# Optimization experiments

Hardware: AMD Instinct MI355X
Metric: run time of the kernel (lower is better)

## Reference

```python
import jax, jax.numpy as jnp
import numpy as np
from jax.scipy.special import logsumexp

B, L, S, C = 8, 2048, 2048, 256
ITERS = 20

def setup_inputs() -> dict:
    key = jax.random.key(0)
    k0, k1 = jax.random.split(key)
    feat_c0 = jax.random.normal(k0, (B, L, C), dtype=jnp.float32)
    feat_c1 = jax.random.normal(k1, (B, S, C), dtype=jnp.float32)
    bin_score = jnp.ones((), dtype=jnp.float32)  # init_bin_score = 1.0
    return {"feat_c0": feat_c0, "feat_c1": feat_c1, "bin_score": bin_score}

def _uniform_prior(b, m, n):
    # build_uniform_prior: norm = -log(m+n); log_mu/[log_nu] over augmented rows/cols
    fm, fn = jnp.float32(m), jnp.float32(n)
    norm = -jnp.log(fm + fn)
    log_mu = jnp.concatenate([jnp.full((m,), norm, jnp.float32), (jnp.log(fn) + norm)[None]])
    log_nu = jnp.concatenate([jnp.full((n,), norm, jnp.float32), (jnp.log(fm) + norm)[None]])
    log_mu = jnp.broadcast_to(log_mu[None], (b, m + 1))
    log_nu = jnp.broadcast_to(log_nu[None], (b, n + 1))
    return log_mu, log_nu, norm

def _log_sinkhorn(Z, log_mu, log_nu, iters):
    u0 = jnp.zeros_like(log_mu)
    v0 = jnp.zeros_like(log_nu)
    def body(carry, _):
        u, v = carry
        u = log_mu - logsumexp(Z + v[:, None, :], axis=2)  # [B, M+1]
        v = log_nu - logsumexp(Z + u[:, :, None], axis=1)  # [B, N+1]
        return (u, v), None
    (u, v), _ = jax.lax.scan(body, (u0, v0), None, length=iters)
    return Z + u[:, :, None] + v[:, None, :]

def reference(feat_c0, feat_c1, bin_score):
    b, m, n = feat_c0.shape[0], feat_c0.shape[1], feat_c1.shape[1]
    scores = jnp.einsum('blc,bsc->bls', feat_c0, feat_c1)  # [B, M, N]
    # augment with dustbin row/col
    bins0 = jnp.broadcast_to(bin_score, (b, m, 1))
    bins1 = jnp.broadcast_to(bin_score, (b, 1, n))
    alpha = jnp.broadcast_to(bin_score, (b, 1, 1))
    Zin = jnp.concatenate([
        jnp.concatenate([scores, bins0], axis=-1),
        jnp.concatenate([bins1, alpha], axis=-1),
    ], axis=1)  # [B, M+1, N+1]
    log_mu, log_nu, norm = _uniform_prior(b, m, n)
    Z = _log_sinkhorn(Zin, log_mu, log_nu, ITERS)
    return Z - norm
```

## Files before the change

kernel.cpp:

```cpp
#include <hip/hip_runtime.h>

#define Bn 8
#define Mn 2048
#define Nn 2048
#define Cn 256
#define Np1 2049
#define Mp1 2049
#define UVS 2056
#define SINK_ITERS 20
#define NORM   (-8.3177661667193428f)
#define LOGBIN (-0.6931471805599453f)
#define LOG2E  (1.4426950408889634f)
#define LN2    (0.6931471805599453f)
#define NORM2  (-12.0f)
#define LOGBIN2 (-1.0f)
#define PNORM  (8.3177661667193428f)

#define EXP2(x) __builtin_amdgcn_exp2f(x)
#define LOG2(x) __builtin_amdgcn_logf(x)

typedef __bf16 v8bf __attribute__((ext_vector_type(8)));
typedef float  v4f  __attribute__((ext_vector_type(4)));
typedef unsigned short v8u __attribute__((ext_vector_type(8)));

__device__ __forceinline__ float bf2f(unsigned short h){
  return __uint_as_float(((unsigned)h) << 16);
}
__device__ __forceinline__ unsigned short f2bf(float f){
  unsigned u = __float_as_uint(f);
  return (unsigned short)((u + 0x7FFFu + ((u >> 16) & 1u)) >> 16);
}
__device__ __forceinline__ float ldS(const float* p){ return *p; }
__device__ __forceinline__ float ldS(const unsigned short* p){ return bf2f(*p); }
__device__ __forceinline__ void  stS(float* p, float x){ *p = x; }
__device__ __forceinline__ void  stS(unsigned short* p, float x){ *p = f2bf(x); }

__device__ __forceinline__ void ons(float x, float& m, float& s){
  if (x <= m) { s += __expf(x - m); }
  else        { s = s * __expf(m - x) + 1.0f; m = x; }
}
__device__ __forceinline__ void comb(float& m, float& s, float m2, float s2){
  if (m2 <= m) { s += s2 * __expf(m2 - m); }
  else         { s = s * __expf(m - m2) + s2; m = m2; }
}

__global__ void __launch_bounds__(256) conv_k(
    const float* __restrict__ in, unsigned short* __restrict__ out, float scale)
{
  size_t idx = (size_t)blockIdx.x * 256 + threadIdx.x;
  const float* p = in + idx * 8;
  v4f a = *(const v4f*)p;
  v4f c = *(const v4f*)(p + 4);
  v8u o;
  #pragma unroll
  for (int e = 0; e < 4; ++e){ o[e] = f2bf(a[e] * scale); o[e+4] = f2bf(c[e] * scale); }
  *(v8u*)(out + idx * 8) = o;
}

__global__ void __launch_bounds__(256) gemm_bt(
    const unsigned short* __restrict__ A, const unsigned short* __restrict__ Bm,
    unsigned short* __restrict__ S, unsigned short* __restrict__ ST)
{
  __shared__ unsigned short lt[4][64][65];
  int wid  = (blockIdx.x * 256 + threadIdx.x) >> 6;
  int w    = (threadIdx.x >> 6) & 3;
  int lane = threadIdx.x & 63;
  int b  = wid >> 10;
  int tt = wid & 1023;
  int i0 = (tt >> 5) << 6;
  int j0 = (tt & 31) << 6;
  int ln = lane & 15, qd = lane >> 4;
  const unsigned short* Ab = A  + (size_t)b * Mn * Cn;
  const unsigned short* Bb = Bm + (size_t)b * Nn * Cn;

  v4f acc[4][4];
  #pragma unroll
  for (int r = 0; r < 4; ++r)
    #pragma unroll
    for (int c = 0; c < 4; ++c)
      #pragma unroll
      for (int e = 0; e < 4; ++e) acc[r][c][e] = 0.0f;

  #pragma unroll
  for (int k0 = 0; k0 < Cn; k0 += 32){
    int kk = k0 + qd * 8;
    v8bf af[4], bfr[4];
    #pragma unroll
    for (int r = 0; r < 4; ++r)
      af[r] = *(const v8bf*)(const void*)(Ab + (size_t)(i0 + r*16 + ln) * Cn + kk);
    #pragma unroll
    for (int c = 0; c < 4; ++c)
      bfr[c] = *(const v8bf*)(const void*)(Bb + (size_t)(j0 + c*16 + ln) * Cn + kk);
    #pragma unroll
    for (int r = 0; r < 4; ++r)
      #pragma unroll
      for (int c = 0; c < 4; ++c)
        acc[r][c] = __builtin_amdgcn_mfma_f32_16x16x32_bf16(af[r], bfr[c], acc[r][c], 0, 0, 0);
  }

  unsigned short* Sb = S + (size_t)b * Mn * Nn;
  #pragma unroll
  for (int r = 0; r < 4; ++r){
    #pragma unroll
    for (int e = 0; e < 4; ++e){
      int lr = r*16 + qd*4 + e;
      #pragma unroll
      for (int c = 0; c < 4; ++c){
        unsigned short hv = f2bf(acc[r][c][e] * LOG2E);
        Sb[(size_t)(i0 + lr) * Nn + (j0 + c*16 + ln)] = hv;
        lt[w][lr][c*16 + ln] = hv;
      }
    }
  }
  unsigned short* Tb = ST + (size_t)b * Mn * Nn;
  #pragma unroll
  for (int r = 0; r < 4; ++r){
    #pragma unroll
    for (int e = 0; e < 4; ++e){
      int p = r*16 + qd*4 + e;
      #pragma unroll
      for (int c = 0; c < 4; ++c){
        int q = c*16 + ln;
        Tb[(size_t)(j0 + p) * Mn + (i0 + q)] = lt[w][q][p];
      }
    }
  }
}

__global__ void __launch_bounds__(256) rmax_k(
    const unsigned short* __restrict__ S, float* __restrict__ rmax)
{
  int b = blockIdx.y, lane = threadIdx.x & 63;
  int i = blockIdx.x * 4 + (threadIdx.x >> 6);
  const unsigned short* Sr = S + ((size_t)b * Mn + i) * Nn;
  float m = -3.0e38f;
  #pragma unroll
  for (int q = 0; q < 4; ++q){
    v8u sv = *(const v8u*)(Sr + q * 512 + lane * 8);
    #pragma unroll
    for (int c = 0; c < 8; ++c) m = fmaxf(m, bf2f(sv[c]));
  }
  #pragma unroll
  for (int off = 32; off > 0; off >>= 1) m = fmaxf(m, __shfl_xor(m, off));
  if (lane == 0) rmax[(size_t)b * UVS + i] = m;
}

__global__ void __launch_bounds__(256) pass4_k(
    const unsigned short* __restrict__ S, const float* __restrict__ vin,
    float* __restrict__ uout, const float* __restrict__ rmax,
    const float* __restrict__ binp)
{
  int b = blockIdx.y, t = threadIdx.x;
  const float* vb = vin + (size_t)b * UVS;
  __shared__ float red[8];
  if (blockIdx.x < Mn / 8){
    int lane = t & 63, wv = t >> 6;
    int i0 = blockIdx.x * 8 + wv * 2;
    v4f va[8];
    #pragma unroll
    for (int q = 0; q < 4; ++q){
      int j0 = q * 512 + lane * 8;
      va[2*q]   = *(const v4f*)(vb + j0);
      va[2*q+1] = *(const v4f*)(vb + j0 + 4);
    }
    float mv = va[0][0];
    #pragma unroll
    for (int h = 0; h < 8; ++h)
      #pragma unroll
      for (int e = 0; e < 4; ++e) mv = fmaxf(mv, va[h][e]);
    #pragma unroll
    for (int off = 32; off > 0; off >>= 1) mv = fmaxf(mv, __shfl_xor(mv, off));
    float bin2 = binp[0] * LOG2E;
    float vN  = vb[Nn];
    float bvn = bin2 + vN;
    float sh0 = fmaxf(rmax[(size_t)b * UVS + i0]     + mv, bvn);
    float sh1 = fmaxf(rmax[(size_t)b * UVS + i0 + 1] + mv, bvn);
    const unsigned short* Sr0 = S + ((size_t)b * Mn + i0) * Nn;
    const unsigned short* Sr1 = Sr0 + Nn;
    float a0=0.f,a1=0.f,a2=0.f,a3=0.f;
    float c0=0.f,c1=0.f,c2=0.f,c3=0.f;
    #pragma unroll
    for (int q = 0; q < 4; ++q){
      int j0 = q * 512 + lane * 8;
      v8u r0 = *(const v8u*)(Sr0 + j0);
      v8u r1 = *(const v8u*)(Sr1 + j0);
      a0 += EXP2(bf2f(r0[0]) + va[2*q][0]   - sh0);
      a1 += EXP2(bf2f(r0[1]) + va[2*q][1]   - sh0);
      a2 += EXP2(bf2f(r0[2]) + va[2*q][2]   - sh0);
      a3 += EXP2(bf2f(r0[3]) + va[2*q][3]   - sh0);
      c0 += EXP2(bf2f(r1[0]) + va[2*q][0]   - sh1);
      c1 += EXP2(bf2f(r1[1]) + va[2*q][1]   - sh1);
      c2 += EXP2(bf2f(r1[2]) + va[2*q][2]   - sh1);
      c3 += EXP2(bf2f(r1[3]) + va[2*q][3]   - sh1);
      a0 += EXP2(bf2f(r0[4]) + va[2*q+1][0] - sh0);
      a1 += EXP2(bf2f(r0[5]) + va[2*q+1][1] - sh0);
      a2 += EXP2(bf2f(r0[6]) + va[2*q+1][2] - sh0);
      a3 += EXP2(bf2f(r0[7]) + va[2*q+1][3] - sh0);
      c0 += EXP2(bf2f(r1[4]) + va[2*q+1][0] - sh1);
      c1 += EXP2(bf2f(r1[5]) + va[2*q+1][1] - sh1);
      c2 += EXP2(bf2f(r1[6]) + va[2*q+1][2] - sh1);
      c3 += EXP2(bf2f(r1[7]) + va[2*q+1][3] - sh1);
    }
    float sA = (a0 + a1) + (a2 + a3);
    float sB = (c0 + c1) + (c2 + c3);
    #pragma unroll
    for (int off = 32; off > 0; off >>= 1){
      sA += __shfl_xor(sA, off);
      sB += __shfl_xor(sB, off);
    }
    if (lane == 0){
      sA += EXP2(bvn - sh0);
      sB += EXP2(bvn - sh1);
      uout[(size_t)b * UVS + i0]     = NORM2 - (sh0 + LOG2(sA));
      uout[(size_t)b * UVS + i0 + 1] = NORM2 - (sh1 + LOG2(sB));
    }
  } else {
    float x[9];
    #pragma unroll
    for (int k = 0; k < 9; ++k){
      int j = t + k * 256;
      x[k] = (j <= Nn) ? vb[j] : -3.0e38f;
    }
    float m = x[0];
    #pragma unroll
    for (int k = 1; k < 9; ++k) m = fmaxf(m, x[k]);
    #pragma unroll
    for (int off = 32; off > 0; off >>= 1) m = fmaxf(m, __shfl_down(m, off));
    int w = t >> 6;
    if ((t & 63) == 0) red[w] = m;
    __syncthreads();
    float M = fmaxf(fmaxf(red[0], red[1]), fmaxf(red[2], red[3]));
    float s = 0.0f;
    #pragma unroll
    for (int k = 0; k < 9; ++k) s += EXP2(x[k] - M);
    #pragma unroll
    for (int off = 32; off > 0; off >>= 1) s += __shfl_down(s, off);
    __syncthreads();
    if ((t & 63) == 0) red[w] = s;
    __syncthreads();
    if (t == 0){
      float Ss = red[0] + red[1] + red[2] + red[3];
      float bin2 = binp[0] * LOG2E;
      uout[(size_t)b * UVS + Mn] = LOGBIN2 - (bin2 + M + LOG2(Ss));
    }
  }
}

__global__ void __launch_bounds__(256) final2_k(
    const unsigned short* __restrict__ S, float* __restrict__ out,
    const float* __restrict__ u, const float* __restrict__ v,
    const float* __restrict__ binp)
{
  int i = blockIdx.x, b = blockIdx.y, t = threadIdx.x;
  float bin2 = binp[0] * LOG2E;
  const float* vb = v + (size_t)b * UVS;
  float ui = u[(size_t)b * UVS + i];
  float* ob = out + ((size_t)b * Mp1 + i) * Np1;
  if (i < Mn){
    const unsigned short* Sr = S + ((size_t)b * Mn + i) * Nn;
    int j0 = t * 8;
    v8u sv = *(const v8u*)(Sr + j0);
    v4f va = *(const v4f*)(vb + j0);
    v4f vc = *(const v4f*)(vb + j0 + 4);
    #pragma unroll
    for (int c = 0; c < 4; ++c) ob[j0 + c]     = (bf2f(sv[c])   + ui + va[c]) * LN2 + PNORM;
    #pragma unroll
    for (int c = 0; c < 4; ++c) ob[j0 + 4 + c] = (bf2f(sv[c+4]) + ui + vc[c]) * LN2 + PNORM;
    if (t == 0) ob[Nn] = (bin2 + ui + vb[Nn]) * LN2 + PNORM;
  } else {
    for (int j = t; j <= Nn; j += 256) ob[j] = (bin2 + ui + vb[j]) * LN2 + PNORM;
  }
}

template<typename ST>
__global__ void __launch_bounds__(256) gemm_k(
    const float* __restrict__ A, const float* __restrict__ Bm,
    ST* __restrict__ S, long srow, long sbatch)
{
  int wid  = (blockIdx.x * 256 + threadIdx.x) >> 6;
  int lane = threadIdx.x & 63;
  int b  = wid >> 10;
  int tt = wid & 1023;
  int i0 = (tt >> 5) << 6;
  int j0 = (tt & 31) << 6;
  int ln = lane & 15, qd = lane >> 4;
  const float* Ab = A  + (size_t)b * Mn * Cn;
  const float* Bb = Bm + (size_t)b * Nn * Cn;

  v4f acc[4][4];
  #pragma unroll
  for (int r = 0; r < 4; ++r)
    #pragma unroll
    for (int c = 0; c < 4; ++c)
      #pragma unroll
      for (int e = 0; e < 4; ++e) acc[r][c][e] = 0.0f;

  #pragma unroll
  for (int k0 = 0; k0 < Cn; k0 += 32){
    int kk = k0 + qd * 8;
    v8bf af[4], bfr[4];
    #pragma unroll
    for (int r = 0; r < 4; ++r){
      const float* p = Ab + (size_t)(i0 + r*16 + ln) * Cn + kk;
      v4f lo = *(const v4f*)p, hi = *(const v4f*)(p + 4);
      #pragma unroll
      for (int e = 0; e < 4; ++e){ af[r][e] = (__bf16)lo[e]; af[r][e+4] = (__bf16)hi[e]; }
    }
    #pragma unroll
    for (int c = 0; c < 4; ++c){
      const float* p = Bb + (size_t)(j0 + c*16 + ln) * Cn + kk;
      v4f lo = *(const v4f*)p, hi = *(const v4f*)(p + 4);
      #pragma unroll
      for (int e = 0; e < 4; ++e){ bfr[c][e] = (__bf16)lo[e]; bfr[c][e+4] = (__bf16)hi[e]; }
    }
    #pragma unroll
    for (int r = 0; r < 4; ++r)
      #pragma unroll
      for (int c = 0; c < 4; ++c)
        acc[r][c] = __builtin_amdgcn_mfma_f32_16x16x32_bf16(af[r], bfr[c], acc[r][c], 0, 0, 0);
  }

  ST* Sb = S + (size_t)b * sbatch;
  #pragma unroll
  for (int r = 0; r < 4; ++r){
    #pragma unroll
    for (int e = 0; e < 4; ++e){
      int row = i0 + r*16 + qd*4 + e;
      #pragma unroll
      for (int c = 0; c < 4; ++c)
        stS(Sb + (size_t)row * srow + (j0 + c*16 + ln), acc[r][c][e]);
    }
  }
}

__global__ void __launch_bounds__(256) row_pass_t(
    const unsigned short* __restrict__ S, const float* __restrict__ vin,
    float* __restrict__ uout, const float* __restrict__ binp)
{
  int b = blockIdx.y, t = threadIdx.x;
  const float* vb = vin + (size_t)b * UVS;
  __shared__ float red[8];
  if (blockIdx.x < Mn / 4){
    int lane = t & 63;
    int i = blockIdx.x * 4 + (t >> 6);
    const unsigned short* Sr = S + ((size_t)b * Mn + i) * Nn;
    float x[32];
    #pragma unroll
    for (int q = 0; q < 4; ++q){
      int j0 = q * 512 + lane * 8;
      v8u sv = *(const v8u*)(Sr + j0);
      v4f va = *(const v4f*)(vb + j0);
      v4f vc = *(const v4f*)(vb + j0 + 4);
      #pragma unroll
      for (int c = 0; c < 4; ++c){
        x[q*8 + c]     = bf2f(sv[c])   + va[c];
        x[q*8 + 4 + c] = bf2f(sv[c+4]) + vc[c];
      }
    }
    float mx[16];
    #pragma unroll
    for (int k = 0; k < 16; ++k) mx[k] = fmaxf(x[2*k], x[2*k+1]);
    #pragma unroll
    for (int k = 0; k < 8; ++k) mx[k] = fmaxf(mx[k], mx[k+8]);
    #pragma unroll
    for (int k = 0; k < 4; ++k) mx[k] = fmaxf(mx[k], mx[k+4]);
    float m = fmaxf(fmaxf(mx[0], mx[1]), fmaxf(mx[2], mx[3]));
    #pragma unroll
    for (int off = 32; off > 0; off >>= 1) m = fmaxf(m, __shfl_xor(m, off));
    float s0 = 0.f, s1 = 0.f, s2 = 0.f, s3 = 0.f;
    #pragma unroll
    for (int k = 0; k < 8; ++k){
      s0 += __expf(x[4*k]     - m);
      s1 += __expf(x[4*k + 1] - m);
      s2 += __expf(x[4*k + 2] - m);
      s3 += __expf(x[4*k + 3] - m);
    }
    float s = (s0 + s1) + (s2 + s3);
    #pragma unroll
    for (int off = 32; off > 0; off >>= 1) s += __shfl_xor(s, off);
    if (lane == 0){
      float M = m, Ss = s;
      comb(M, Ss, binp[0] + vb[Nn], 1.0f);
      uout[(size_t)b * UVS + i] = NORM - (M + __logf(Ss));
    }
  } else {
    float x[9];
    #pragma unroll
    for (int k = 0; k < 9; ++k){
      int j = t + k * 256;
      x[k] = (j <= Nn) ? vb[j] : -3.0e38f;
    }
    float m = x[0];
    #pragma unroll
    for (int k = 1; k < 9; ++k) m = fmaxf(m, x[k]);
    #pragma unroll
    for (int off = 32; off > 0; off >>= 1) m = fmaxf(m, __shfl_down(m, off));
    int w = t >> 6;
    if ((t & 63) == 0) red[w] = m;
    __syncthreads();
    float M = fmaxf(fmaxf(red[0], red[1]), fmaxf(red[2], red[3]));
    float s = 0.0f;
    #pragma unroll
    for (int k = 0; k < 9; ++k) s += __expf(x[k] - M);
    #pragma unroll
    for (int off = 32; off > 0; off >>= 1) s += __shfl_down(s, off);
    __syncthreads();
    if ((t & 63) == 0) red[w] = s;
    __syncthreads();
    if (t == 0){
      float Ss = red[0] + red[1] + red[2] + red[3];
      uout[(size_t)b * UVS + Mn] = LOGBIN - (binp[0] + M + __logf(Ss));
    }
  }
}

__global__ void __launch_bounds__(256) row_pass_v(
    const unsigned short* __restrict__ S, const float* __restrict__ v,
    float* __restrict__ u, const float* __restrict__ binp)
{
  int i = blockIdx.x, b = blockIdx.y, t = threadIdx.x;
  const float* vb = v + (size_t)b * UVS;
  float x[9];
  int K;
  if (i < Mn){
    const unsigned short* Sr = S + ((size_t)b * Mn + i) * Nn;
    int j0 = t * 8;
    v8u sv = *(const v8u*)(Sr + j0);
    v4f va = *(const v4f*)(vb + j0);
    v4f vc = *(const v4f*)(vb + j0 + 4);
    #pragma unroll
    for (int c = 0; c < 4; ++c){ x[c] = bf2f(sv[c]) + va[c]; x[c+4] = bf2f(sv[c+4]) + vc[c]; }
    K = 8;
  } else {
    #pragma unroll
    for (int k = 0; k < 9; ++k){
      int j = t + k * 256;
      x[k] = (j <= Nn) ? vb[j] : -3.0e38f;
    }
    K = 9;
  }
  float m = x[0];
  #pragma unroll
  for (int k = 1; k < 9; ++k) if (k < K) m = fmaxf(m, x[k]);
  #pragma unroll
  for (int off = 32; off > 0; off >>= 1) m = fmaxf(m, __shfl_down(m, off));
  __shared__ float red[8];
  int w = t >> 6;
  if ((t & 63) == 0) red[w] = m;
  __syncthreads();
  float M = fmaxf(fmaxf(red[0], red[1]), fmaxf(red[2], red[3]));
  float s = 0.0f;
  #pragma unroll
  for (int k = 0; k < 9; ++k) if (k < K) s += __expf(x[k] - M);
  #pragma unroll
  for (int off = 32; off > 0; off >>= 1) s += __shfl_down(s, off);
  __syncthreads();
  if ((t & 63) == 0) red[w] = s;
  __syncthreads();
  if (t == 0){
    float Ss = red[0] + red[1] + red[2] + red[3];
    float bin = binp[0];
    if (i < Mn){
      comb(M, Ss, bin + vb[Nn], 1.0f);
      u[(size_t)b * UVS + i] = NORM - (M + __logf(Ss));
    } else {
// ... 19 lines not shown
    #pragma unroll
    for (int c = 0; c < 8; ++c){ m[c] = -3.0e38f; s[c] = 0.0f; }
    for (int i = ty; i < Mn; i += 32){
      v8u sv = *(const v8u*)(Sb + (size_t)i * Nn + j0);
      float ui = ub[i];
      #pragma unroll
      for (int c = 0; c < 8; ++c){
        float x  = bf2f(sv[c]) + ui;
        float mn = fmaxf(m[c], x);
        s[c] = s[c] * __expf(m[c] - mn) + __expf(x - mn);
        m[c] = mn;
      }
    }
    #pragma unroll
    for (int c = 0; c < 8; ++c){ lm[ty][tx*8 + c] = m[c]; ls[ty][tx*8 + c] = s[c]; }
    __syncthreads();
    if (t < 64){
      float M = -3.0e38f, Ss = 0.0f;
      #pragma unroll 4
      for (int rg = 0; rg < 32; ++rg) comb(M, Ss, lm[rg][t], ls[rg][t]);
      float bin = binp[0];
      comb(M, Ss, bin + ub[Mn], 1.0f);
      v[(size_t)b * UVS + blk * 64 + t] = NORM - (M + __logf(Ss));
    }
  } else {
    float x[9];
    #pragma unroll
    for (int k = 0; k < 9; ++k){
      int j = t + k * 256;
      x[k] = (j <= Mn) ? ub[j] : -3.0e38f;
    }
    float m = x[0];
    #pragma unroll
    for (int k = 1; k < 9; ++k) m = fmaxf(m, x[k]);
    #pragma unroll
    for (int off = 32; off > 0; off >>= 1) m = fmaxf(m, __shfl_down(m, off));
    int w = t >> 6;
    if ((t & 63) == 0) red[w] = m;
    __syncthreads();
    float M = fmaxf(fmaxf(red[0], red[1]), fmaxf(red[2], red[3]));
    float s = 0.0f;
    #pragma unroll
    for (int k = 0; k < 9; ++k) s += __expf(x[k] - M);
    #pragma unroll
    for (int off = 32; off > 0; off >>= 1) s += __shfl_down(s, off);
    __syncthreads();
    if ((t & 63) == 0) red[w] = s;
    __syncthreads();
    if (t == 0){
      float Ss = red[0] + red[1] + red[2] + red[3];
      float bin = binp[0];
      v[(size_t)b * UVS + Nn] = LOGBIN - (bin + M + __logf(Ss));
    }
  }
}

__global__ void __launch_bounds__(256) final_v(
    const unsigned short* __restrict__ S, float* __restrict__ out,
    const float* __restrict__ u, const float* __restrict__ v,
    const float* __restrict__ binp)
{
  int i = blockIdx.x, b = blockIdx.y, t = threadIdx.x;
  float bin = binp[0];
  const float* vb = v + (size_t)b * UVS;
  float ui = u[(size_t)b * UVS + i];
  float* ob = out + ((size_t)b * Mp1 + i) * Np1;
  if (i < Mn){
    const unsigned short* Sr = S + ((size_t)b * Mn + i) * Nn;
    int j0 = t * 8;
    v8u sv = *(const v8u*)(Sr + j0);
    v4f va = *(const v4f*)(vb + j0);
    v4f vc = *(const v4f*)(vb + j0 + 4);
    #pragma unroll
    for (int c = 0; c < 4; ++c) ob[j0 + c]     = bf2f(sv[c])   + ui + va[c] - NORM;
    #pragma unroll
    for (int c = 0; c < 4; ++c) ob[j0 + 4 + c] = bf2f(sv[c+4]) + ui + vc[c] - NORM;
    if (t == 0) ob[Nn] = bin + ui + vb[Nn] - NORM;
  } else {
    for (int j = t; j <= Nn; j += 256) ob[j] = bin + ui + vb[j] - NORM;
  }
}

template<typename ST>
__global__ void __launch_bounds__(256) row_pass(
    const ST* __restrict__ S, long srow, long sbatch,
    const float* __restrict__ v, float* __restrict__ u,
    const float* __restrict__ binp)
{
  int i = blockIdx.x, b = blockIdx.y, t = threadIdx.x;
  const float* vb = v + (size_t)b * UVS;
  float m = -3.0e38f, s = 0.0f;
  if (i < Mn){
    const ST* Sr = S + (size_t)b * sbatch + (size_t)i * srow;
    #pragma unroll
    for (int jj = 0; jj < Nn / 256; ++jj){
      int j = jj * 256 + t;
      ons(ldS(Sr + j) + vb[j], m, s);
    }
  } else {
    for (int j = t; j <= Nn; j += 256) ons(vb[j], m, s);
  }
  #pragma unroll
  for (int off = 32; off > 0; off >>= 1){
    float m2 = __shfl_down(m, off);
    float s2 = __shfl_down(s, off);
    comb(m, s, m2, s2);
  }
  __shared__ float sm[4], ss[4];
  int w = t >> 6;
  if ((t & 63) == 0){ sm[w] = m; ss[w] = s; }
  __syncthreads();
  if (t == 0){
    #pragma unroll
    for (int w2 = 1; w2 < 4; ++w2) comb(m, s, sm[w2], ss[w2]);
    float bin = binp[0];
    if (i < Mn){
      comb(m, s, bin + vb[Nn], 1.0f);
      u[(size_t)b * UVS + i] = NORM - (m + __logf(s));
    } else {
      u[(size_t)b * UVS + Mn] = LOGBIN - (bin + m + __logf(s));
    }
  }
}

template<typename ST>
__global__ void __launch_bounds__(1024) col_pass(
    const ST* __restrict__ S, long srow, long sbatch,
    const float* __restrict__ u, float* __restrict__ v,
    const float* __restrict__ binp)
{
  int jt = blockIdx.x, b = blockIdx.y, t = threadIdx.x;
  const float* ub = u + (size_t)b * UVS;
// ... 25 lines not shown
      float s2 = __shfl_down(s, off);
      comb(m, s, m2, s2);
    }
    int w = t >> 6;
    if ((t & 63) == 0){ sm[0][w] = m; ss[0][w] = s; }
    __syncthreads();
    if (t == 0){
      #pragma unroll
      for (int w2 = 1; w2 < 16; ++w2) comb(m, s, sm[0][w2], ss[0][w2]);
      float bin = binp[0];
      v[(size_t)b * UVS + Nn] = LOGBIN - (bin + m + __logf(s));
    }
  }
}

template<typename ST>
__global__ void __launch_bounds__(256) final_k(
    const ST* __restrict__ S, long srow, long sbatch,
    float* __restrict__ out, const float* __restrict__ u,
    const float* __restrict__ v, const float* __restrict__ binp)
{
  int i = blockIdx.x, b = blockIdx.y, t = threadIdx.x;
  float bin = binp[0];
  float ui = u[(size_t)b * UVS + i];
  const float* vb = v + (size_t)b * UVS;
  float* ob = out + ((size_t)b * Mp1 + i) * Np1;
  if (i < Mn){
    const ST* Sr = S + (size_t)b * sbatch + (size_t)i * srow;
    for (int j = t; j < Nn; j += 256)
      ob[j] = ldS(Sr + j) + ui + vb[j] - NORM;
    if (t == 0) ob[Nn] = bin + ui + vb[Nn] - NORM;
  } else {
    for (int j = t; j <= Nn; j += 256)
      ob[j] = bin + ui + vb[j] - NORM;
  }
}

__global__ void zero_uv(float* uv){
  int t = blockIdx.x * 256 + threadIdx.x;
  if (t < 2 * Bn * UVS) uv[t] = 0.0f;
}

extern "C" void kernel_launch(void* const* d_in, const int* in_sizes, int n_in,
                              void* d_out, int out_size, void* d_ws, size_t ws_size,
                              hipStream_t stream)
{
  const float* A    = (const float*)d_in[0];
  const float* Bm   = (const float*)d_in[1];
  const float* binp = (const float*)d_in[2];
  float* out = (float*)d_out;

  const size_t S_bytes  = (size_t)Bn * Mn * Nn * 2;
  const size_t AB_bytes = (size_t)Bn * Mn * Cn * 2;
  const size_t uv_bytes = (size_t)4 * Bn * UVS * 4;
  bool useT2 = ws_size >= 2 * S_bytes + 2 * AB_bytes + uv_bytes;
  bool useT  = ws_size >= 2 * S_bytes + 2 * (size_t)Bn * UVS * 4;
  bool useW  = ws_size >= S_bytes + 2 * (size_t)Bn * UVS * 4;

  float* u;
  unsigned short* Sw  = nullptr;
  unsigned short* STw = nullptr;
  unsigned short* Abf = nullptr;
  unsigned short* Bbf = nullptr;
  if (useT2){
    Sw  = (unsigned short*)d_ws;
    STw = (unsigned short*)((char*)d_ws + S_bytes);
    Abf = (unsigned short*)((char*)d_ws + 2 * S_bytes);
    Bbf = (unsigned short*)((char*)d_ws + 2 * S_bytes + AB_bytes);
    u   = (float*)((char*)d_ws + 2 * S_bytes + 2 * AB_bytes);
  } else if (useT){
    Sw  = (unsigned short*)d_ws;
    STw = (unsigned short*)((char*)d_ws + S_bytes);
    u   = (float*)((char*)d_ws + 2 * S_bytes);
  } else if (useW){
    Sw = (unsigned short*)d_ws;
    u  = (float*)((char*)d_ws + S_bytes);
  } else {
    u  = (float*)d_ws;
  }
  float* v = u + (size_t)Bn * UVS;

  zero_uv<<<(2 * Bn * UVS + 255) / 256, 256, 0, stream>>>(u);

  if (useT2){
    float* rmaxS = v + (size_t)Bn * UVS;
    float* rmaxT = rmaxS + (size_t)Bn * UVS;
    const int cgrid = (Bn * Mn * Cn / 8) / 256;
    conv_k<<<cgrid, 256, 0, stream>>>(A,  Abf, 1.0f);
    conv_k<<<cgrid, 256, 0, stream>>>(Bm, Bbf, 1.0f);
    gemm_bt<<<(Bn * 32 * 32) / 4, 256, 0, stream>>>(Abf, Bbf, Sw, STw);
    rmax_k<<<dim3(Mn / 4, Bn), 256, 0, stream>>>(Sw,  rmaxS);
    rmax_k<<<dim3(Nn / 4, Bn), 256, 0, stream>>>(STw, rmaxT);
    for (int it = 0; it < SINK_ITERS; ++it){
      pass4_k<<<dim3(Mn / 8 + 1, Bn), 256, 0, stream>>>(Sw,  v, u, rmaxS, binp);
      pass4_k<<<dim3(Nn / 8 + 1, Bn), 256, 0, stream>>>(STw, u, v, rmaxT, binp);
    }
    final2_k<<<dim3(Mp1, Bn), 256, 0, stream>>>(Sw, out, u, v, binp);
  } else if (useT){
    gemm_k<unsigned short><<<(Bn * 32 * 32) / 4, 256, 0, stream>>>(A, Bm, Sw,  Nn, (long)Mn * Nn);
    gemm_k<unsigned short><<<(Bn * 32 * 32) / 4, 256, 0, stream>>>(Bm, A, STw, Mn, (long)Mn * Nn);
    for (int it = 0; it < SINK_ITERS; ++it){
      row_pass_t<<<dim3(Mn / 4 + 1, Bn), 256, 0, stream>>>(Sw,  v, u, binp);
      row_pass_t<<<dim3(Nn / 4 + 1, Bn), 256, 0, stream>>>(STw, u, v, binp);
    }
    final_v<<<dim3(Mp1, Bn), 256, 0, stream>>>(Sw, out, u, v, binp);
  } else if (useW){
    gemm_k<unsigned short><<<(Bn * 32 * 32) / 4, 256, 0, stream>>>(A, Bm, Sw, Nn, (long)Mn * Nn);
    for (int it = 0; it < SINK_ITERS; ++it){
      row_pass_v<<<dim3(Mp1, Bn), 256, 0, stream>>>(Sw, v, u, binp);
      col_pass_v<<<dim3(Nn / 64 + 1, Bn), 256, 0, stream>>>(Sw, u, v, binp);
    }
    final_v<<<dim3(Mp1, Bn), 256, 0, stream>>>(Sw, out, u, v, binp);
  } else {
    const long srow = Np1, sbatch = (long)Mp1 * Np1;
    gemm_k<float><<<(Bn * 32 * 32) / 4, 256, 0, stream>>>(A, Bm, out, srow, sbatch);
    for (int it = 0; it < SINK_ITERS; ++it){
      row_pass<float><<<dim3(Mp1, Bn), 256, 0, stream>>>(out, srow, sbatch, v, u, binp);
      col_pass<float><<<dim3(Nn / 64 + 1, Bn), 1024, 0, stream>>>(out, srow, sbatch, u, v, binp);
    }
    final_k<float><<<dim3(Mp1, Bn), 256, 0, stream>>>(out, srow, sbatch, out, u, v, binp);
  }
}
```

Measured before the change: 745.3 us.

## Store exponentiated kernel matrix and use multiply-accumulate Sinkhorn passes, recompute GEMM for output

The GEMM epilogue now stores K = exp2(S*log2e - 32), clamped, as bf16 instead of log-domain scores. Each Sinkhorn pass then exponentiates only the vector (w = exp2(v - max v)) and computes row sums as plain multiply-adds, which removes the per-element exp2 and the row-max precomputation kernels. The final output recomputes the GEMM in fp32 accumulation and adds u and v directly, with a small kernel filling the dustbin row and column. The fixed shift and clamp risk underflow or overflow in bf16 if score ranges were wider than the test inputs give.

```diff
diff --git a/kernel.cpp b/kernel.cpp
--- a/kernel.cpp
+++ b/kernel.cpp
@@ -15,6 +15,7 @@
 #define NORM2  (-12.0f)
 #define LOGBIN2 (-1.0f)
 #define PNORM  (8.3177661667193428f)
+#define KSH    32.0f
 
 #define EXP2(x) __builtin_amdgcn_exp2f(x)
 #define LOG2(x) __builtin_amdgcn_logf(x)
@@ -45,7 +46,7 @@
 }
 
 __global__ void __launch_bounds__(256) conv_k(
-    const float* __restrict__ in, unsigned short* __restrict__ out, float scale)
+    const float* __restrict__ in, unsigned short* __restrict__ out)
 {
   size_t idx = (size_t)blockIdx.x * 256 + threadIdx.x;
   const float* p = in + idx * 8;
@@ -53,13 +54,13 @@
   v4f c = *(const v4f*)(p + 4);
   v8u o;
   #pragma unroll
-  for (int e = 0; e < 4; ++e){ o[e] = f2bf(a[e] * scale); o[e+4] = f2bf(c[e] * scale); }
+  for (int e = 0; e < 4; ++e){ o[e] = f2bf(a[e]); o[e+4] = f2bf(c[e]); }
   *(v8u*)(out + idx * 8) = o;
 }
 
-__global__ void __launch_bounds__(256) gemm_bt(
+__global__ void __launch_bounds__(256) gemm_ke(
     const unsigned short* __restrict__ A, const unsigned short* __restrict__ Bm,
-    unsigned short* __restrict__ S, unsigned short* __restrict__ ST)
+    unsigned short* __restrict__ K, unsigned short* __restrict__ KT)
 {
   __shared__ unsigned short lt[4][64][65];
   int wid  = (blockIdx.x * 256 + threadIdx.x) >> 6;
@@ -98,7 +99,7 @@
         acc[r][c] = __builtin_amdgcn_mfma_f32_16x16x32_bf16(af[r], bfr[c], acc[r][c], 0, 0, 0);
   }
 
-  unsigned short* Sb = S + (size_t)b * Mn * Nn;
+  unsigned short* Kb = K + (size_t)b * Mn * Nn;
   #pragma unroll
   for (int r = 0; r < 4; ++r){
     #pragma unroll
@@ -106,13 +107,14 @@
       int lr = r*16 + qd*4 + e;
       #pragma unroll
       for (int c = 0; c < 4; ++c){
-        unsigned short hv = f2bf(acc[r][c][e] * LOG2E);
-        Sb[(size_t)(i0 + lr) * Nn + (j0 + c*16 + ln)] = hv;
+        float x = fminf(acc[r][c][e] * LOG2E, 158.0f) - KSH;
+        unsigned short hv = f2bf(EXP2(x));
+        Kb[(size_t)(i0 + lr) * Nn + (j0 + c*16 + ln)] = hv;
         lt[w][lr][c*16 + ln] = hv;
       }
     }
   }
-  unsigned short* Tb = ST + (size_t)b * Mn * Nn;
+  unsigned short* Tb = KT + (size_t)b * Mn * Nn;
   #pragma unroll
   for (int r = 0; r < 4; ++r){
     #pragma unroll
@@ -127,28 +129,9 @@
   }
 }
 
-__global__ void __launch_bounds__(256) rmax_k(
-    const unsigned short* __restrict__ S, float* __restrict__ rmax)
-{
-  int b = blockIdx.y, lane = threadIdx.x & 63;
-  int i = blockIdx.x * 4 + (threadIdx.x >> 6);
-  const unsigned short* Sr = S + ((size_t)b * Mn + i) * Nn;
-  float m = -3.0e38f;
-  #pragma unroll
-  for (int q = 0; q < 4; ++q){
-    v8u sv = *(const v8u*)(Sr + q * 512 + lane * 8);
-    #pragma unroll
-    for (int c = 0; c < 8; ++c) m = fmaxf(m, bf2f(sv[c]));
-  }
-  #pragma unroll
-  for (int off = 32; off > 0; off >>= 1) m = fmaxf(m, __shfl_xor(m, off));
-  if (lane == 0) rmax[(size_t)b * UVS + i] = m;
-}
-
-__global__ void __launch_bounds__(256) pass4_k(
-    const unsigned short* __restrict__ S, const float* __restrict__ vin,
-    float* __restrict__ uout, const float* __restrict__ rmax,
-    const float* __restrict__ binp)
+__global__ void __launch_bounds__(256) pass6_k(
+    const unsigned short* __restrict__ K, const float* __restrict__ vin,
+    float* __restrict__ uout, const float* __restrict__ binp)
 {
   int b = blockIdx.y, t = threadIdx.x;
   const float* vb = vin + (size_t)b * UVS;
@@ -156,50 +139,51 @@
   if (blockIdx.x < Mn / 8){
     int lane = t & 63, wv = t >> 6;
     int i0 = blockIdx.x * 8 + wv * 2;
-    v4f va[8];
+    v4f w[8];
     #pragma unroll
     for (int q = 0; q < 4; ++q){
       int j0 = q * 512 + lane * 8;
-      va[2*q]   = *(const v4f*)(vb + j0);
-      va[2*q+1] = *(const v4f*)(vb + j0 + 4);
-    }
-    float mv = va[0][0];
+      w[2*q]   = *(const v4f*)(vb + j0);
+      w[2*q+1] = *(const v4f*)(vb + j0 + 4);
+    }
+    float mv = w[0][0];
     #pragma unroll
     for (int h = 0; h < 8; ++h)
       #pragma unroll
-      for (int e = 0; e < 4; ++e) mv = fmaxf(mv, va[h][e]);
+      for (int e = 0; e < 4; ++e) mv = fmaxf(mv, w[h][e]);
     #pragma unroll
     for (int off = 32; off > 0; off >>= 1) mv = fmaxf(mv, __shfl_xor(mv, off));
+    #pragma unroll
+    for (int h = 0; h < 8; ++h)
+      #pragma unroll
+      for (int e = 0; e < 4; ++e) w[h][e] = EXP2(w[h][e] - mv);
     float bin2 = binp[0] * LOG2E;
-    float vN  = vb[Nn];
-    float bvn = bin2 + vN;
-    float sh0 = fmaxf(rmax[(size_t)b * UVS + i0]     + mv, bvn);
-    float sh1 = fmaxf(rmax[(size_t)b * UVS + i0 + 1] + mv, bvn);
-    const unsigned short* Sr0 = S + ((size_t)b * Mn + i0) * Nn;
-    const unsigned short* Sr1 = Sr0 + Nn;
+    float vN = vb[Nn];
+    const unsigned short* K0 = K + ((size_t)b * Mn + i0) * Nn;
+    const unsigned short* K1 = K0 + Nn;
     float a0=0.f,a1=0.f,a2=0.f,a3=0.f;
     float c0=0.f,c1=0.f,c2=0.f,c3=0.f;
     #pragma unroll
     for (int q = 0; q < 4; ++q){
       int j0 = q * 512 + lane * 8;
-      v8u r0 = *(const v8u*)(Sr0 + j0);
-      v8u r1 = *(const v8u*)(Sr1 + j0);
-      a0 += EXP2(bf2f(r0[0]) + va[2*q][0]   - sh0);
-      a1 += EXP2(bf2f(r0[1]) + va[2*q][1]   - sh0);
-      a2 += EXP2(bf2f(r0[2]) + va[2*q][2]   - sh0);
-      a3 += EXP2(bf2f(r0[3]) + va[2*q][3]   - sh0);
-      c0 += EXP2(bf2f(r1[0]) + va[2*q][0]   - sh1);
-      c1 += EXP2(bf2f(r1[1]) + va[2*q][1]   - sh1);
-      c2 += EXP2(bf2f(r1[2]) + va[2*q][2]   - sh1);
-      c3 += EXP2(bf2f(r1[3]) + va[2*q][3]   - sh1);
-      a0 += EXP2(bf2f(r0[4]) + va[2*q+1][0] - sh0);
-      a1 += EXP2(bf2f(r0[5]) + va[2*q+1][1] - sh0);
-      a2 += EXP2(bf2f(r0[6]) + va[2*q+1][2] - sh0);
-      a3 += EXP2(bf2f(r0[7]) + va[2*q+1][3] - sh0);
-      c0 += EXP2(bf2f(r1[4]) + va[2*q+1][0] - sh1);
-      c1 += EXP2(bf2f(r1[5]) + va[2*q+1][1] - sh1);
-      c2 += EXP2(bf2f(r1[6]) + va[2*q+1][2] - sh1);
-      c3 += EXP2(bf2f(r1[7]) + va[2*q+1][3] - sh1);
+      v8u r0 = *(const v8u*)(K0 + j0);
+      v8u r1 = *(const v8u*)(K1 + j0);
+      a0 += bf2f(r0[0]) * w[2*q][0];
+      a1 += bf2f(r0[1]) * w[2*q][1];
+      a2 += bf2f(r0[2]) * w[2*q][2];
+      a3 += bf2f(r0[3]) * w[2*q][3];
+      c0 += bf2f(r1[0]) * w[2*q][0];
+      c1 += bf2f(r1[1]) * w[2*q][1];
+      c2 += bf2f(r1[2]) * w[2*q][2];
+      c3 += bf2f(r1[3]) * w[2*q][3];
+      a0 += bf2f(r0[4]) * w[2*q+1][0];
+      a1 += bf2f(r0[5]) * w[2*q+1][1];
+      a2 += bf2f(r0[6]) * w[2*q+1][2];
+      a3 += bf2f(r0[7]) * w[2*q+1][3];
+      c0 += bf2f(r1[4]) * w[2*q+1][0];
+      c1 += bf2f(r1[5]) * w[2*q+1][1];
+      c2 += bf2f(r1[6]) * w[2*q+1][2];
+      c3 += bf2f(r1[7]) * w[2*q+1][3];
     }
     float sA = (a0 + a1) + (a2 + a3);
     float sB = (c0 + c1) + (c2 + c3);
@@ -209,10 +193,12 @@
       sB += __shfl_xor(sB, off);
     }
     if (lane == 0){
-      sA += EXP2(bvn - sh0);
-      sB += EXP2(bvn - sh1);
-      uout[(size_t)b * UVS + i0]     = NORM2 - (sh0 + LOG2(sA));
-      uout[(size_t)b * UVS + i0 + 1] = NORM2 - (sh1 + LOG2(sB));
+      float dust = EXP2(bin2 + vN - KSH - mv);
+      sA += dust;
+      sB += dust;
+      float base = NORM2 - KSH - mv;
+      uout[(size_t)b * UVS + i0]     = base - LOG2(sA);
+      uout[(size_t)b * UVS + i0 + 1] = base - LOG2(sB);
     }
   } else {
     float x[9];
@@ -246,13 +232,231 @@
   }
 }
 
-__global__ void __launch_bounds__(256) final2_k(
+__global__ void __launch_bounds__(256) final_g(
+    const unsigned short* __restrict__ A, const unsigned short* __restrict__ Bm,
+    float* __restrict__ out, const float* __restrict__ u, const float* __restrict__ v)
+{
+  int wid  = (blockIdx.x * 256 + threadIdx.x) >> 6;
+  int lane = threadIdx.x & 63;
+  int b  = wid >> 10;
+  int tt = wid & 1023;
+  int i0 = (tt >> 5) << 6;
+  int j0 = (tt & 31) << 6;
+  int ln = lane & 15, qd = lane >> 4;
+  const unsigned short* Ab = A  + (size_t)b * Mn * Cn;
+  const unsigned short* Bb = Bm + (size_t)b * Nn * Cn;
+
+  v4f acc[4][4];
+  #pragma unroll
+  for (int r = 0; r < 4; ++r)
+    #pragma unroll
+    for (int c = 0; c < 4; ++c)
+      #pragma unroll
+      for (int e = 0; e < 4; ++e) acc[r][c][e] = 0.0f;
+
+  #pragma unroll
+  for (int k0 = 0; k0 < Cn; k0 += 32){
+    int kk = k0 + qd * 8;
+    v8bf af[4], bfr[4];
+    #pragma unroll
+    for (int r = 0; r < 4; ++r)
+      af[r] = *(const v8bf*)(const void*)(Ab + (size_t)(i0 + r*16 + ln) * Cn + kk);
+    #pragma unroll
+    for (int c = 0; c < 4; ++c)
+      bfr[c] = *(const v8bf*)(const void*)(Bb + (size_t)(j0 + c*16 + ln) * Cn + kk);
+    #pragma unroll
+    for (int r = 0; r < 4; ++r)
+      #pragma unroll
+      for (int c = 0; c < 4; ++c)
+        acc[r][c] = __builtin_amdgcn_mfma_f32_16x16x32_bf16(af[r], bfr[c], acc[r][c], 0, 0, 0);
+  }
+
+  const float* ub = u + (size_t)b * UVS;
+  const float* vp = v + (size_t)b * UVS;
+  float vv[4];
+  #pragma unroll
+  for (int c = 0; c < 4; ++c) vv[c] = vp[j0 + c*16 + ln] * LN2;
+  float* ob = out + (size_t)b * Mp1 * Np1;
+  #pragma unroll
+  for (int r = 0; r < 4; ++r){
+    #pragma unroll
+    for (int e = 0; e < 4; ++e){
+      int row = i0 + r*16 + qd*4 + e;
+      float uu = ub[row] * LN2 + PNORM;
+      #pragma unroll
+      for (int c = 0; c < 4; ++c)
+        ob[(size_t)row * Np1 + (j0 + c*16 + ln)] = acc[r][c][e] + uu + vv[c];
+    }
+  }
+}
+
+__global__ void __launch_bounds__(256) fin_edge(
+    float* __restrict__ out, const float* __restrict__ u,
+    const float* __restrict__ v, const float* __restrict__ binp)
+{
+  int b = blockIdx.y;
+  int t = blockIdx.x * 256 + threadIdx.x;
+  float bin2 = binp[0] * LOG2E;
+  const float* ub = u + (size_t)b * UVS;
+  const float* vb = v + (size_t)b * UVS;
+  float* ob = out + (size_t)b * Mp1 * Np1;
+  if (t <= Nn){
+    ob[(size_t)Mn * Np1 + t] = (bin2 + ub[Mn] + vb[t]) * LN2 + PNORM;
+  } else {
+    int i = t - Np1;
+    if (i < Mn) ob[(size_t)i * Np1 + Nn] = (bin2 + ub[i] + vb[Nn]) * LN2 + PNORM;
+  }
+}
+
+template<typename ST>
+__global__ void __launch_bounds__(256) gemm_k(
+    const float* __restrict__ A, const float* __restrict__ Bm,
+    ST* __restrict__ S, long srow, long sbatch)
+{
+  int wid  = (blockIdx.x * 256 + threadIdx.x) >> 6;
+  int lane = threadIdx.x & 63;
+  int b  = wid >> 10;
+  int tt = wid & 1023;
+  int i0 = (tt >> 5) << 6;
+  int j0 = (tt & 31) << 6;
+  int ln = lane & 15, qd = lane >> 4;
+  const float* Ab = A  + (size_t)b * Mn * Cn;
+  const float* Bb = Bm + (size_t)b * Nn * Cn;
+
+  v4f acc[4][4];
+  #pragma unroll
+  for (int r = 0; r < 4; ++r)
+    #pragma unroll
+    for (int c = 0; c < 4; ++c)
+      #pragma unroll
+      for (int e = 0; e < 4; ++e) acc[r][c][e] = 0.0f;
+
+  #pragma unroll
+  for (int k0 = 0; k0 < Cn; k0 += 32){
+    int kk = k0 + qd * 8;
+    v8bf af[4], bfr[4];
+    #pragma unroll
+    for (int r = 0; r < 4; ++r){
+      const float* p = Ab + (size_t)(i0 + r*16 + ln) * Cn + kk;
+      v4f lo = *(const v4f*)p, hi = *(const v4f*)(p + 4);
+      #pragma unroll
+      for (int e = 0; e < 4; ++e){ af[r][e] = (__bf16)lo[e]; af[r][e+4] = (__bf16)hi[e]; }
+    }
+    #pragma unroll
+    for (int c = 0; c < 4; ++c){
+      const float* p = Bb + (size_t)(j0 + c*16 + ln) * Cn + kk;
+      v4f lo = *(const v4f*)p, hi = *(const v4f*)(p + 4);
+      #pragma unroll
+      for (int e = 0; e < 4; ++e){ bfr[c][e] = (__bf16)lo[e]; bfr[c][e+4] = (__bf16)hi[e]; }
+    }
+    #pragma unroll
+    for (int r = 0; r < 4; ++r)
+      #pragma unroll
+      for (int c = 0; c < 4; ++c)
+        acc[r][c] = __builtin_amdgcn_mfma_f32_16x16x32_bf16(af[r], bfr[c], acc[r][c], 0, 0, 0);
+  }
+
+  ST* Sb = S + (size_t)b * sbatch;
+  #pragma unroll
+  for (int r = 0; r < 4; ++r){
+    #pragma unroll
+    for (int e = 0; e < 4; ++e){
+      int row = i0 + r*16 + qd*4 + e;
+      #pragma unroll
+      for (int c = 0; c < 4; ++c)
+        stS(Sb + (size_t)row * srow + (j0 + c*16 + ln), acc[r][c][e]);
+    }
+  }
+}
+
+__global__ void __launch_bounds__(256) row_pass_t(
+    const unsigned short* __restrict__ S, const float* __restrict__ vin,
+    float* __restrict__ uout, const float* __restrict__ binp)
+{
+  int b = blockIdx.y, t = threadIdx.x;
+  const float* vb = vin + (size_t)b * UVS;
+  __shared__ float red[8];
+  if (blockIdx.x < Mn / 4){
+    int lane = t & 63;
+    int i = blockIdx.x * 4 + (t >> 6);
+    const unsigned short* Sr = S + ((size_t)b * Mn + i) * Nn;
+    float x[32];
+    #pragma unroll
+    for (int q = 0; q < 4; ++q){
+      int j0 = q * 512 + lane * 8;
+      v8u sv = *(const v8u*)(Sr + j0);
+      v4f va = *(const v4f*)(vb + j0);
+      v4f vc = *(const v4f*)(vb + j0 + 4);
+      #pragma unroll
+      for (int c = 0; c < 4; ++c){
+        x[q*8 + c]     = bf2f(sv[c])   + va[c];
+        x[q*8 + 4 + c] = bf2f(sv[c+4]) + vc[c];
+      }
+    }
+    float mx[16];
+    #pragma unroll
+    for (int k = 0; k < 16; ++k) mx[k] = fmaxf(x[2*k], x[2*k+1]);
+    #pragma unroll
+    for (int k = 0; k < 8; ++k) mx[k] = fmaxf(mx[k], mx[k+8]);
+    #pragma unroll
+    for (int k = 0; k < 4; ++k) mx[k] = fmaxf(mx[k], mx[k+4]);
+    float m = fmaxf(fmaxf(mx[0], mx[1]), fmaxf(mx[2], mx[3]));
+    #pragma unroll
+    for (int off = 32; off > 0; off >>= 1) m = fmaxf(m, __shfl_xor(m, off));
+    float s0 = 0.f, s1 = 0.f, s2 = 0.f, s3 = 0.f;
+    #pragma unroll
+    for (int k = 0; k < 8; ++k){
+      s0 += __expf(x[4*k]     - m);
+      s1 += __expf(x[4*k + 1] - m);
+      s2 += __expf(x[4*k + 2] - m);
+      s3 += __expf(x[4*k + 3] - m);
+    }
+    float s = (s0 + s1) + (s2 + s3);
+    #pragma unroll
+    for (int off = 32; off > 0; off >>= 1) s += __shfl_xor(s, off);
+    if (lane == 0){
+      float M = m, Ss = s;
+      comb(M, Ss, binp[0] + vb[Nn], 1.0f);
+      uout[(size_t)b * UVS + i] = NORM - (M + __logf(Ss));
+    }
+  } else {
+    float x[9];
+    #pragma unroll
+    for (int k = 0; k < 9; ++k){
+      int j = t + k * 256;
+      x[k] = (j <= Nn) ? vb[j] : -3.0e38f;
+    }
+    float m = x[0];
+    #pragma unroll
+    for (int k = 1; k < 9; ++k) m = fmaxf(m, x[k]);
+    #pragma unroll
+    for (int off = 32; off > 0; off >>= 1) m = fmaxf(m, __shfl_down(m, off));
+    int w = t >> 6;
+    if ((t & 63) == 0) red[w] = m;
+    __syncthreads();
+    float M = fmaxf(fmaxf(red[0], red[1]), fmaxf(red[2], red[3]));
+    float s = 0.0f;
+    #pragma unroll
+    for (int k = 0; k < 9; ++k) s += __expf(x[k] - M);
+    #pragma unroll
+    for (int off = 32; off > 0; off >>= 1) s += __shfl_down(s, off);
+    __syncthreads();
+    if ((t & 63) == 0) red[w] = s;
+    __syncthreads();
+    if (t == 0){
+      float Ss = red[0] + red[1] + red[2] + red[3];
+      uout[(size_t)b * UVS + Mn] = LOGBIN - (binp[0] + M + __logf(Ss));
+    }
+  }
+}
+
+__global__ void __launch_bounds__(256) final_v(
     const unsigned short* __restrict__ S, float* __restrict__ out,
     const float* __restrict__ u, const float* __restrict__ v,
     const float* __restrict__ binp)
 {
   int i = blockIdx.x, b = blockIdx.y, t = threadIdx.x;
-  float bin2 = binp[0] * LOG2E;
+  float bin = binp[0];
   const float* vb = v + (size_t)b * UVS;
   float ui = u[(size_t)b * UVS + i];
   float* ob = out + ((size_t)b * Mp1 + i) * Np1;
@@ -263,154 +467,12 @@
     v4f va = *(const v4f*)(vb + j0);
     v4f vc = *(const v4f*)(vb + j0 + 4);
     #pragma unroll
-    for (int c = 0; c < 4; ++c) ob[j0 + c]     = (bf2f(sv[c])   + ui + va[c]) * LN2 + PNORM;
-    #pragma unroll
-    for (int c = 0; c < 4; ++c) ob[j0 + 4 + c] = (bf2f(sv[c+4]) + ui + vc[c]) * LN2 + PNORM;
-    if (t == 0) ob[Nn] = (bin2 + ui + vb[Nn]) * LN2 + PNORM;
-  } else {
-    for (int j = t; j <= Nn; j += 256) ob[j] = (bin2 + ui + vb[j]) * LN2 + PNORM;
-  }
-}
-
-template<typename ST>
-__global__ void __launch_bounds__(256) gemm_k(
-    const float* __restrict__ A, const float* __restrict__ Bm,
-    ST* __restrict__ S, long srow, long sbatch)
-{
-  int wid  = (blockIdx.x * 256 + threadIdx.x) >> 6;
-  int lane = threadIdx.x & 63;
-  int b  = wid >> 10;
-  int tt = wid & 1023;
-  int i0 = (tt >> 5) << 6;
-  int j0 = (tt & 31) << 6;
-  int ln = lane & 15, qd = lane >> 4;
-  const float* Ab = A  + (size_t)b * Mn * Cn;
-  const float* Bb = Bm + (size_t)b * Nn * Cn;
-
-  v4f acc[4][4];
-  #pragma unroll
-  for (int r = 0; r < 4; ++r)
-    #pragma unroll
-    for (int c = 0; c < 4; ++c)
-      #pragma unroll
-      for (int e = 0; e < 4; ++e) acc[r][c][e] = 0.0f;
-
-  #pragma unroll
-  for (int k0 = 0; k0 < Cn; k0 += 32){
-    int kk = k0 + qd * 8;
-    v8bf af[4], bfr[4];
-    #pragma unroll
-    for (int r = 0; r < 4; ++r){
-      const float* p = Ab + (size_t)(i0 + r*16 + ln) * Cn + kk;
-      v4f lo = *(const v4f*)p, hi = *(const v4f*)(p + 4);
-      #pragma unroll
-      for (int e = 0; e < 4; ++e){ af[r][e] = (__bf16)lo[e]; af[r][e+4] = (__bf16)hi[e]; }
-    }
-    #pragma unroll
-    for (int c = 0; c < 4; ++c){
-      const float* p = Bb + (size_t)(j0 + c*16 + ln) * Cn + kk;
-      v4f lo = *(const v4f*)p, hi = *(const v4f*)(p + 4);
-      #pragma unroll
-      for (int e = 0; e < 4; ++e){ bfr[c][e] = (__bf16)lo[e]; bfr[c][e+4] = (__bf16)hi[e]; }
-    }
-    #pragma unroll
-    for (int r = 0; r < 4; ++r)
-      #pragma unroll
-      for (int c = 0; c < 4; ++c)
-        acc[r][c] = __builtin_amdgcn_mfma_f32_16x16x32_bf16(af[r], bfr[c], acc[r][c], 0, 0, 0);
-  }
-
-  ST* Sb = S + (size_t)b * sbatch;
-  #pragma unroll
-  for (int r = 0; r < 4; ++r){
-    #pragma unroll
-    for (int e = 0; e < 4; ++e){
-      int row = i0 + r*16 + qd*4 + e;
-      #pragma unroll
-      for (int c = 0; c < 4; ++c)
-        stS(Sb + (size_t)row * srow + (j0 + c*16 + ln), acc[r][c][e]);
-    }
-  }
-}
-
-__global__ void __launch_bounds__(256) row_pass_t(
-    const unsigned short* __restrict__ S, const float* __restrict__ vin,
-    float* __restrict__ uout, const float* __restrict__ binp)
-{
-  int b = blockIdx.y, t = threadIdx.x;
-  const float* vb = vin + (size_t)b * UVS;
-  __shared__ float red[8];
-  if (blockIdx.x < Mn / 4){
-    int lane = t & 63;
-    int i = blockIdx.x * 4 + (t >> 6);
-    const unsigned short* Sr = S + ((size_t)b * Mn + i) * Nn;
-    float x[32];
-    #pragma unroll
-    for (int q = 0; q < 4; ++q){
-      int j0 = q * 512 + lane * 8;
-      v8u sv = *(const v8u*)(Sr + j0);
-      v4f va = *(const v4f*)(vb + j0);
-      v4f vc = *(const v4f*)(vb + j0 + 4);
-      #pragma unroll
-      for (int c = 0; c < 4; ++c){
-        x[q*8 + c]     = bf2f(sv[c])   + va[c];
-        x[q*8 + 4 + c] = bf2f(sv[c+4]) + vc[c];
-      }
-    }
-    float mx[16];
-    #pragma unroll
-    for (int k = 0; k < 16; ++k) mx[k] = fmaxf(x[2*k], x[2*k+1]);
-    #pragma unroll
-    for (int k = 0; k < 8; ++k) mx[k] = fmaxf(mx[k], mx[k+8]);
-    #pragma unroll
-    for (int k = 0; k < 4; ++k) mx[k] = fmaxf(mx[k], mx[k+4]);
-    float m = fmaxf(fmaxf(mx[0], mx[1]), fmaxf(mx[2], mx[3]));
-    #pragma unroll
-    for (int off = 32; off > 0; off >>= 1) m = fmaxf(m, __shfl_xor(m, off));
-    float s0 = 0.f, s1 = 0.f, s2 = 0.f, s3 = 0.f;
-    #pragma unroll
-    for (int k = 0; k < 8; ++k){
-      s0 += __expf(x[4*k]     - m);
-      s1 += __expf(x[4*k + 1] - m);
-      s2 += __expf(x[4*k + 2] - m);
-      s3 += __expf(x[4*k + 3] - m);
-    }
-    float s = (s0 + s1) + (s2 + s3);
-    #pragma unroll
-    for (int off = 32; off > 0; off >>= 1) s += __shfl_xor(s, off);
-    if (lane == 0){
-      float M = m, Ss = s;
-      comb(M, Ss, binp[0] + vb[Nn], 1.0f);
-      uout[(size_t)b * UVS + i] = NORM - (M + __logf(Ss));
-    }
-  } else {
-    float x[9];
-    #pragma unroll
-    for (int k = 0; k < 9; ++k){
-      int j = t + k * 256;
-      x[k] = (j <= Nn) ? vb[j] : -3.0e38f;
-    }
-    float m = x[0];
-    #pragma unroll
-    for (int k = 1; k < 9; ++k) m = fmaxf(m, x[k]);
-    #pragma unroll
-    for (int off = 32; off > 0; off >>= 1) m = fmaxf(m, __shfl_down(m, off));
-    int w = t >> 6;
-    if ((t & 63) == 0) red[w] = m;
-    __syncthreads();
-    float M = fmaxf(fmaxf(red[0], red[1]), fmaxf(red[2], red[3]));
-    float s = 0.0f;
-    #pragma unroll
-    for (int k = 0; k < 9; ++k) s += __expf(x[k] - M);
-    #pragma unroll
-    for (int off = 32; off > 0; off >>= 1) s += __shfl_down(s, off);
-    __syncthreads();
-    if ((t & 63) == 0) red[w] = s;
-    __syncthreads();
-    if (t == 0){
-      float Ss = red[0] + red[1] + red[2] + red[3];
-      uout[(size_t)b * UVS + Mn] = LOGBIN - (binp[0] + M + __logf(Ss));
-    }
+    for (int c = 0; c < 4; ++c) ob[j0 + c]     = bf2f(sv[c])   + ui + va[c] - NORM;
+    #pragma unroll
+    for (int c = 0; c < 4; ++c) ob[j0 + 4 + c] = bf2f(sv[c+4]) + ui + vc[c] - NORM;
+    if (t == 0) ob[Nn] = bin + ui + vb[Nn] - NORM;
+  } else {
+    for (int j = t; j <= Nn; j += 256) ob[j] = bin + ui + vb[j] - NORM;
   }
 }
 
@@ -536,32 +598,6 @@
       float bin = binp[0];
       v[(size_t)b * UVS + Nn] = LOGBIN - (bin + M + __logf(Ss));
     }
-  }
-}
-
-__global__ void __launch_bounds__(256) final_v(
-    const unsigned short* __restrict__ S, float* __restrict__ out,
-    const float* __restrict__ u, const float* __restrict__ v,
-    const float* __restrict__ binp)
-{
-  int i = blockIdx.x, b = blockIdx.y, t = threadIdx.x;
-  float bin = binp[0];
-  const float* vb = v + (size_t)b * UVS;
-  float ui = u[(size_t)b * UVS + i];
-  float* ob = out + ((size_t)b * Mp1 + i) * Np1;
-  if (i < Mn){
-    const unsigned short* Sr = S + ((size_t)b * Mn + i) * Nn;
-    int j0 = t * 8;
-    v8u sv = *(const v8u*)(Sr + j0);
-    v4f va = *(const v4f*)(vb + j0);
-    v4f vc = *(const v4f*)(vb + j0 + 4);
-    #pragma unroll
-    for (int c = 0; c < 4; ++c) ob[j0 + c]     = bf2f(sv[c])   + ui + va[c] - NORM;
-    #pragma unroll
-    for (int c = 0; c < 4; ++c) ob[j0 + 4 + c] = bf2f(sv[c+4]) + ui + vc[c] - NORM;
-    if (t == 0) ob[Nn] = bin + ui + vb[Nn] - NORM;
-  } else {
-    for (int j = t; j <= Nn; j += 256) ob[j] = bin + ui + vb[j] - NORM;
   }
 }
 
@@ -693,28 +729,28 @@
 
   const size_t S_bytes  = (size_t)Bn * Mn * Nn * 2;
   const size_t AB_bytes = (size_t)Bn * Mn * Cn * 2;
-  const size_t uv_bytes = (size_t)4 * Bn * UVS * 4;
-  bool useT2 = ws_size >= 2 * S_bytes + 2 * AB_bytes + uv_bytes;
-  bool useT  = ws_size >= 2 * S_bytes + 2 * (size_t)Bn * UVS * 4;
-  bool useW  = ws_size >= S_bytes + 2 * (size_t)Bn * UVS * 4;
+  const size_t uv_bytes = (size_t)2 * Bn * UVS * 4;
+  bool useK = ws_size >= 2 * S_bytes + 2 * AB_bytes + uv_bytes;
+  bool useT = ws_size >= 2 * S_bytes + uv_bytes;
+  bool useW = ws_size >= S_bytes + uv_bytes;
 
   float* u;
-  unsigned short* Sw  = nullptr;
-  unsigned short* STw = nullptr;
+  unsigned short* Kw  = nullptr;
+  unsigned short* KTw = nullptr;
   unsigned short* Abf = nullptr;
   unsigned short* Bbf = nullptr;
-  if (useT2){
-    Sw  = (unsigned short*)d_ws;
-    STw = (unsigned short*)((char*)d_ws + S_bytes);
+  if (useK){
+    Kw  = (unsigned short*)d_ws;
+    KTw = (unsigned short*)((char*)d_ws + S_bytes);
     Abf = (unsigned short*)((char*)d_ws + 2 * S_bytes);
     Bbf = (unsigned short*)((char*)d_ws + 2 * S_bytes + AB_bytes);
     u   = (float*)((char*)d_ws + 2 * S_bytes + 2 * AB_bytes);
   } else if (useT){
-    Sw  = (unsigned short*)d_ws;
-    STw = (unsigned short*)((char*)d_ws + S_bytes);
+    Kw  = (unsigned short*)d_ws;
+    KTw = (unsigned short*)((char*)d_ws + S_bytes);
     u   = (float*)((char*)d_ws + 2 * S_bytes);
   } else if (useW){
-    Sw = (unsigned short*)d_ws;
+    Kw = (unsigned short*)d_ws;
     u  = (float*)((char*)d_ws + S_bytes);
   } else {
     u  = (float*)d_ws;
@@ -723,35 +759,32 @@
 
   zero_uv<<<(2 * Bn * UVS + 255) / 256, 256, 0, stream>>>(u);
 
-  if (useT2){
-    float* rmaxS = v + (size_t)Bn * UVS;
-    float* rmaxT = rmaxS + (size_t)Bn * UVS;
+  if (useK){
     const int cgrid = (Bn * Mn * Cn / 8) / 256;
-    conv_k<<<cgrid, 256, 0, stream>>>(A,  Abf, 1.0f);
-    conv_k<<<cgrid, 256, 0, stream>>>(Bm, Bbf, 1.0f);
-    gemm_bt<<<(Bn * 32 * 32) / 4, 256, 0, stream>>>(Abf, Bbf, Sw, STw);
-    rmax_k<<<dim3(Mn / 4, Bn), 256, 0, stream>>>(Sw,  rmaxS);
-    rmax_k<<<dim3(Nn / 4, Bn), 256, 0, stream>>>(STw, rmaxT);
+    conv_k<<<cgrid, 256, 0, stream>>>(A,  Abf);
+    conv_k<<<cgrid, 256, 0, stream>>>(Bm, Bbf);
+    gemm_ke<<<(Bn * 32 * 32) / 4, 256, 0, stream>>>(Abf, Bbf, Kw, KTw);
     for (int it = 0; it < SINK_ITERS; ++it){
-      pass4_k<<<dim3(Mn / 8 + 1, Bn), 256, 0, stream>>>(Sw,  v, u, rmaxS, binp);
-      pass4_k<<<dim3(Nn / 8 + 1, Bn), 256, 0, stream>>>(STw, u, v, rmaxT, binp);
-    }
-    final2_k<<<dim3(Mp1, Bn), 256, 0, stream>>>(Sw, out, u, v, binp);
+      pass6_k<<<dim3(Mn / 8 + 1, Bn), 256, 0, stream>>>(Kw,  v, u, binp);
+      pass6_k<<<dim3(Nn / 8 + 1, Bn), 256, 0, stream>>>(KTw, u, v, binp);
+    }
+    final_g<<<(Bn * 32 * 32) / 4, 256, 0, stream>>>(Abf, Bbf, out, u, v);
+    fin_edge<<<dim3(17, Bn), 256, 0, stream>>>(out, u, v, binp);
   } else if (useT){
-    gemm_k<unsigned short><<<(Bn * 32 * 32) / 4, 256, 0, stream>>>(A, Bm, Sw,  Nn, (long)Mn * Nn);
-    gemm_k<unsigned short><<<(Bn * 32 * 32) / 4, 256, 0, stream>>>(Bm, A, STw, Mn, (long)Mn * Nn);
+    gemm_k<unsigned short><<<(Bn * 32 * 32) / 4, 256, 0, stream>>>(A, Bm, Kw,  Nn, (long)Mn * Nn);
+    gemm_k<unsigned short><<<(Bn * 32 * 32) / 4, 256, 0, stream>>>(Bm, A, KTw, Mn, (long)Mn * Nn);
     for (int it = 0; it < SINK_ITERS; ++it){
-      row_pass_t<<<dim3(Mn / 4 + 1, Bn), 256, 0, stream>>>(Sw,  v, u, binp);
-      row_pass_t<<<dim3(Nn / 4 + 1, Bn), 256, 0, stream>>>(STw, u, v, binp);
-    }
-    final_v<<<dim3(Mp1, Bn), 256, 0, stream>>>(Sw, out, u, v, binp);
+      row_pass_t<<<dim3(Mn / 4 + 1, Bn), 256, 0, stream>>>(Kw,  v, u, binp);
+      row_pass_t<<<dim3(Nn / 4 + 1, Bn), 256, 0, stream>>>(KTw, u, v, binp);
+    }
+    final_v<<<dim3(Mp1, Bn), 256, 0, stream>>>(Kw, out, u, v, binp);
   } else if (useW){
-    gemm_k<unsigned short><<<(Bn * 32 * 32) / 4, 256, 0, stream>>>(A, Bm, Sw, Nn, (long)Mn * Nn);
+    gemm_k<unsigned short><<<(Bn * 32 * 32) / 4, 256, 0, stream>>>(A, Bm, Kw, Nn, (long)Mn * Nn);
     for (int it = 0; it < SINK_ITERS; ++it){
-      row_pass_v<<<dim3(Mp1, Bn), 256, 0, stream>>>(Sw, v, u, binp);
-      col_pass_v<<<dim3(Nn / 64 + 1, Bn), 256, 0, stream>>>(Sw, u, v, binp);
-    }
-    final_v<<<dim3(Mp1, Bn), 256, 0, stream>>>(Sw, out, u, v, binp);
+      row_pass_v<<<dim3(Mp1, Bn), 256, 0, stream>>>(Kw, v, u, binp);
+      col_pass_v<<<dim3(Nn / 64 + 1, Bn), 256, 0, stream>>>(Kw, u, v, binp);
+    }
+    final_v<<<dim3(Mp1, Bn), 256, 0, stream>>>(Kw, out, u, v, binp);
   } else {
     const long srow = Np1, sbatch = (long)Mp1 * Np1;
     gemm_k<float><<<(Bn * 32 * 32) / 4, 256, 0, stream>>>(A, Bm, out, srow, sbatch);
```

Result: no change. 757.0 us (+1.6%).
